# Kernel tuning notes

Hardware: AMD Instinct MI355X
Metric: run time of the kernel (lower is better)

## Reference

```python
import jax, jax.numpy as jnp
import numpy as np

K = 20
EPS = 1e-5

def _lrelu(x):
    return jnp.where(x >= 0, x, 0.2 * x)

def _bn(x, g, b, m, v, axis=1):
    shp = [1] * x.ndim
    shp[axis] = -1
    scale = (g / jnp.sqrt(v + EPS)).reshape(shp)
    return (x - m.reshape(shp)) * scale + b.reshape(shp)

def _graph_feature(x, k):
    # x: [B, C, N] -> [B, 2C, N, k]  (kNN in feature space, concat(x_j - x_i, x_i))
    xx = jnp.sum(x * x, axis=1)                        # [B, N]
    inner = jnp.einsum('bcn,bcm->bnm', x, x)           # [B, N, N]
    neg_dist = 2.0 * inner - xx[:, :, None] - xx[:, None, :]
    _, idx = jax.lax.top_k(neg_dist, k)                # [B, N, k] nearest neighbors
    xt = jnp.transpose(x, (0, 2, 1))                   # [B, N, C]
    nb = jax.vmap(lambda f, i: f[i])(xt, idx)          # [B, N, k, C]
    center = jnp.broadcast_to(xt[:, :, None, :], nb.shape)
    feat = jnp.concatenate([nb - center, center], axis=-1)  # [B, N, k, 2C]
    return jnp.transpose(feat, (0, 3, 1, 2))

def _edge_block(x, w, g, b, m, v):
    # EdgeConv: graph feature -> 1x1 conv -> BN -> LeakyReLU -> max over k
    f = _graph_feature(x, K)                           # [B, 2C, N, k]
    y = jnp.einsum('oc,bcnk->bonk', w, f)
    y = _lrelu(_bn(y, g, b, m, v, 1))
    return jnp.max(y, axis=-1)                         # [B, O, N]


def setup_inputs() -> dict:
    key = jax.random.key(0)
    ks = iter(jax.random.split(key, 64))
    def randn(*s, scale=1.0):
        return jax.random.normal(next(ks), s, dtype=jnp.float32) * scale
    def unif(*s):
        return jax.random.uniform(next(ks), s, dtype=jnp.float32, minval=0.5, maxval=1.5)
    d = {}
    d['x'] = randn(16, 3, 1024)
    # conv / linear weights (fan-in scaled)
    for name, o, c in [('w1', 64, 6), ('w2', 64, 128), ('w3', 128, 128),
                       ('w4', 256, 256), ('w5', 1024, 512),
                       ('wl1', 512, 2048), ('wl2', 256, 512), ('wl3', 101, 256)]:
        d[name] = randn(o, c, scale=1.0 / np.sqrt(c))
    d['bl2'] = randn(256, scale=0.02)
    d['bl3'] = randn(101, scale=0.02)
    # BN params (eval-mode running stats)
    for i, c in [('1', 64), ('2', 64), ('3', 128), ('4', 256), ('5', 1024), ('6', 512), ('7', 256)]:
        d['g' + i] = 1.0 + randn(c, scale=0.1)
        d['b' + i] = randn(c, scale=0.1)
        d['m' + i] = randn(c, scale=0.1)
        d['v' + i] = unif(c)
    return d


def reference(x, w1, g1, b1, m1, v1, w2, g2, b2, m2, v2, w3, g3, b3, m3, v3,
              w4, g4, b4, m4, v4, w5, g5, b5, m5, v5,
              wl1, g6, b6, m6, v6, wl2, bl2, g7, b7, m7, v7, wl3, bl3):
    x1 = _edge_block(x,  w1, g1, b1, m1, v1)   # [B, 64, N]
    x2 = _edge_block(x1, w2, g2, b2, m2, v2)   # [B, 64, N]
    x3 = _edge_block(x2, w3, g3, b3, m3, v3)   # [B, 128, N]
    x4 = _edge_block(x3, w4, g4, b4, m4, v4)   # [B, 256, N]
    xc = jnp.concatenate([x1, x2, x3, x4], axis=1)           # [B, 512, N]
    y = _lrelu(_bn(jnp.einsum('oc,bcn->bon', w5, xc), g5, b5, m5, v5, 1))  # [B, 1024, N]
    p = jnp.concatenate([jnp.max(y, axis=-1), jnp.mean(y, axis=-1)], axis=1)  # [B, 2048]
    h = _lrelu(_bn(p @ wl1.T, g6, b6, m6, v6, 1))            # [B, 512]
    h = _lrelu(_bn(h @ wl2.T + bl2, g7, b7, m7, v7, 1))      # [B, 256]
    return h @ wl3.T + bl3                                   # [B, 101]
```

## Files before the change

kernel.cpp:

```cpp
#include <hip/hip_runtime.h>
#include <cstdint>
#include <cmath>

#define DI __device__ __forceinline__

constexpr int BB = 16;
constexpr int NN = 1024;
constexpr int KK = 20;
constexpr int NPT = BB*NN;
constexpr float EPSF = 1e-5f;
constexpr float NEGINF = -3.0e38f;

DI float lrelu(float x){ return x >= 0.f ? x : 0.2f * x; }
DI float dot4(const float4 a, const float4 b){ return a.x*b.x + a.y*b.y + a.z*b.z + a.w*b.w; }
DI unsigned short f2bf(float x){
    uint32_t u = __float_as_uint(x);
    uint32_t r = (u + 0x7fffu + ((u >> 16) & 1u)) >> 16;
    return (unsigned short)r;
}

DI float wave_max64(float v){
    v = fmaxf(v, __int_as_float(__builtin_amdgcn_mov_dpp(__float_as_int(v), 0x121, 0xF, 0xF, true)));
    v = fmaxf(v, __int_as_float(__builtin_amdgcn_mov_dpp(__float_as_int(v), 0x122, 0xF, 0xF, true)));
    v = fmaxf(v, __int_as_float(__builtin_amdgcn_mov_dpp(__float_as_int(v), 0x124, 0xF, 0xF, true)));
    v = fmaxf(v, __int_as_float(__builtin_amdgcn_mov_dpp(__float_as_int(v), 0x128, 0xF, 0xF, true)));
    v = fmaxf(v, __shfl_xor(v, 16));
    v = fmaxf(v, __shfl_xor(v, 32));
    return v;
}

typedef __attribute__((ext_vector_type(8))) short short8v;
typedef __attribute__((ext_vector_type(4))) float f32x4;

__global__ void k_transpose(const float* __restrict__ x, float* __restrict__ xt)
{
    int i = blockIdx.x * 256 + threadIdx.x;
    if (i >= NPT) return;
    int b = i >> 10, n = i & 1023;
    #pragma unroll
    for (int c = 0; c < 3; ++c) xt[i*3 + c] = x[(b*3 + c)*NN + n];
}

__global__ void k_sqnorm(const float* __restrict__ src, int stride, int C, float* __restrict__ xx)
{
    int i = blockIdx.x * 256 + threadIdx.x;
    if (i >= NPT) return;
    const float* r = src + (size_t)i * stride;
    float s = 0.f;
    for (int c = 0; c < C; ++c){ float v = r[c]; s += v * v; }
    xx[i] = s;
}

template<int C>
__global__ __launch_bounds__(1024, 4) void k_knn(const float* __restrict__ src, int stride,
                                                 const float* __restrict__ xx,
                                                 int* __restrict__ idxo)
{
    constexpr bool SMALL = (C == 3);
    constexpr int CG = SMALL ? 1 : (C / 4);
    constexpr int TS = SMALL ? 5 : C;
    constexpr int NBUF = SMALL ? 1 : 2;
    constexpr int LPT = SMALL ? 1 : (128*CG/1024);
    __shared__ float tile[NBUF][128 * TS];

    const int tid  = threadIdx.x;
    const int lane = tid & 63;
    const int wv   = __builtin_amdgcn_readfirstlane(tid >> 6);
    const int b  = blockIdx.x >> 4;
    const int q0 = (blockIdx.x & 15) << 6;
    const int qbase = b*NN + q0 + (wv << 2);

    const float* qp0 = src + (size_t)(qbase + 0)*stride;
    const float* qp1 = src + (size_t)(qbase + 1)*stride;
    const float* qp2 = src + (size_t)(qbase + 2)*stride;
    const float* qp3 = src + (size_t)(qbase + 3)*stride;

    float xxq[4];
    #pragma unroll
    for (int q = 0; q < 4; ++q) xxq[q] = xx[qbase + q];

    float val[4][16];

    if constexpr (SMALL){
        #pragma unroll
        for (int t = 0; t < 8; ++t){
            __syncthreads();
            for (int i = tid; i < 128*3; i += 1024){
                int row = i / 3, c = i % 3;
                tile[0][row*TS + c] = src[(size_t)(b*NN + t*128 + row)*stride + c];
            }
            __syncthreads();
            float c0a = tile[0][lane*TS+0], c0b = tile[0][lane*TS+1], c0c = tile[0][lane*TS+2];
            float c1a = tile[0][(64+lane)*TS+0], c1b = tile[0][(64+lane)*TS+1], c1c = tile[0][(64+lane)*TS+2];
            float q00 = qp0[0], q01 = qp0[1], q02 = qp0[2];
            float q10 = qp1[0], q11 = qp1[1], q12 = qp1[2];
            float q20 = qp2[0], q21 = qp2[1], q22 = qp2[2];
            float q30 = qp3[0], q31 = qp3[1], q32 = qp3[2];
            float xxm0 = xx[b*NN + t*128 + lane];
            float xxm1 = xx[b*NN + t*128 + 64 + lane];
            val[0][2*t]   = 2.f*(q00*c0a + q01*c0b + q02*c0c) - xxq[0] - xxm0;
            val[0][2*t+1] = 2.f*(q00*c1a + q01*c1b + q02*c1c) - xxq[0] - xxm1;
            val[1][2*t]   = 2.f*(q10*c0a + q11*c0b + q12*c0c) - xxq[1] - xxm0;
            val[1][2*t+1] = 2.f*(q10*c1a + q11*c1b + q12*c1c) - xxq[1] - xxm1;
            val[2][2*t]   = 2.f*(q20*c0a + q21*c0b + q22*c0c) - xxq[2] - xxm0;
            val[2][2*t+1] = 2.f*(q20*c1a + q21*c1b + q22*c1c) - xxq[2] - xxm1;
            val[3][2*t]   = 2.f*(q30*c0a + q31*c0b + q32*c0c) - xxq[3] - xxm0;
            val[3][2*t+1] = 2.f*(q30*c1a + q31*c1b + q32*c1c) - xxq[3] - xxm1;
        }
    } else {
        float4 nx[LPT];
        #pragma unroll
        for (int k = 0; k < LPT; ++k){
            int i = tid + k*1024;
            int row = i / CG, cg = i % CG;
            nx[k] = *(const float4*)(src + (size_t)(b*NN + row)*stride + cg*4);
        }
        #pragma unroll
        for (int k = 0; k < LPT; ++k){
            int i = tid + k*1024;
            int row = i / CG, cg = i % CG;
            int p = cg ^ (row & (CG - 1));
            *(float4*)(&tile[0][row*TS + p*4]) = nx[k];
        }

        for (int t = 0; t < 8; ++t){
            __syncthreads();
            if (t < 7){
                #pragma unroll
                for (int k = 0; k < LPT; ++k){
                    int i = tid + k*1024;
                    int row = i / CG, cg = i % CG;
                    nx[k] = *(const float4*)(src + (size_t)(b*NN + (t+1)*128 + row)*stride + cg*4);
                }
            }
            const float* tb = tile[t & 1];

            float acc[4][2];
            #pragma unroll
            for (int q = 0; q < 4; ++q){ acc[q][0] = 0.f; acc[q][1] = 0.f; }
            const int sw = lane & (CG - 1);
            #pragma unroll 2
            for (int cg0 = 0; cg0 < CG; ++cg0){
                float4 cf0 = *(const float4*)(tb + lane*TS      + ((cg0 ^ sw) << 2));
                float4 cf1 = *(const float4*)(tb + (64+lane)*TS + ((cg0 ^ sw) << 2));
                float4 qf0 = *(const float4*)(qp0 + (cg0 << 2));
                float4 qf1 = *(const float4*)(qp1 + (cg0 << 2));
                float4 qf2 = *(const float4*)(qp2 + (cg0 << 2));
                float4 qf3 = *(const float4*)(qp3 + (cg0 << 2));
                acc[0][0] += dot4(qf0, cf0); acc[0][1] += dot4(qf0, cf1);
                acc[1][0] += dot4(qf1, cf0); acc[1][1] += dot4(qf1, cf1);
                acc[2][0] += dot4(qf2, cf0); acc[2][1] += dot4(qf2, cf1);
                acc[3][0] += dot4(qf3, cf0); acc[3][1] += dot4(qf3, cf1);
            }
            float xxm0 = xx[b*NN + t*128 + lane];
            float xxm1 = xx[b*NN + t*128 + 64 + lane];
            #pragma unroll
            for (int q = 0; q < 4; ++q){
                val[q][2*t]   = 2.f*acc[q][0] - xxq[q] - xxm0;
                val[q][2*t+1] = 2.f*acc[q][1] - xxq[q] - xxm1;
            }

            if (t < 7){
                float* wb = &tile[(t+1) & 1][0];
                #pragma unroll
                for (int k = 0; k < LPT; ++k){
                    int i = tid + k*1024;
                    int row = i / CG, cg = i % CG;
                    int p = cg ^ (row & (CG - 1));
                    *(float4*)(&wb[row*TS + p*4]) = nx[k];
                }
            }
        }
    }

    #pragma unroll
    for (int q = 0; q < 4; ++q){
        const int orow = (qbase + q) * KK;

        float s[16];
        #pragma unroll
        for (int j = 0; j < 16; ++j) s[j] = val[q][j];
        #pragma unroll
        for (int k = 2; k <= 16; k <<= 1){
            #pragma unroll
            for (int jj = k >> 1; jj > 0; jj >>= 1){
                #pragma unroll
                for (int i = 0; i < 16; ++i){
                    int l = i ^ jj;
                    if (l > i){
                        float a = s[i], c = s[l];
                        float mx = fmaxf(a, c), mn = fminf(a, c);
                        bool up = ((i & k) == 0);
                        s[i] = up ? mx : mn;
                        s[l] = up ? mn : mx;
                    }
                }
            }
        }

        float T = NEGINF;
        for (int it = 0; it < 21; ++it){
            float m = wave_max64(s[0]);
            T = m;
            unsigned long long mk = __ballot(s[0] == m);
            int wl = __ffsll(mk) - 1;
            bool adv = (lane == wl);
            #pragma unroll
            for (int j = 0; j < 15; ++j) s[j] = adv ? s[j+1] : s[j];
            s[15] = adv ? NEGINF : s[15];
        }

        int cnt = 0;
        #pragma unroll
        for (int j = 0; j < 16; ++j) cnt += (val[q][j] > T) ? 1 : 0;
        int off = cnt;
        #pragma unroll
        for (int d = 1; d < 64; d <<= 1){
            int tt = __shfl_up(off, d);
            if (lane >= d) off += tt;
        }
        int total = __shfl(off, 63);
        int pos = orow + off - cnt;
        #pragma unroll
        for (int j = 0; j < 16; ++j){
            if (val[q][j] > T){ idxo[pos] = j*64 + lane; ++pos; }
        }
        if (total < KK){
            int rem = KK - total;
            int prior = 0;
            #pragma unroll
            for (int j = 0; j < 16; ++j){
                unsigned long long mk = __ballot(val[q][j] == T);
                int below = __popcll(mk & ((1ull << lane) - 1ull));
                if ((val[q][j] == T) && (prior + below < rem))
                    idxo[orow + total + prior + below] = j*64 + lane;
                prior += __popcll(mk);
            }
        }
    }
}

__global__ void k_wprep(const float* __restrict__ w, int O, int C, float* __restrict__ wp)
{
    int i = blockIdx.x*256 + threadIdx.x;
    if (i >= O*C) return;
    int o = i / C, c = i % C;
    float a = w[o*2*C + c];
    float bq = w[o*2*C + C + c];
    wp[o*C + c]       = a;
    wp[(O + o)*C + c] = bq - a;
}

template<int K, int M2, int O, bool UB16>
__global__ __launch_bounds__(256) void k_uvgemm(const float* __restrict__ srcp,
    const float* __restrict__ wp,
    const float* __restrict__ g, const float* __restrict__ bp,
    const float* __restrict__ mp, const float* __restrict__ vp,
    float* __restrict__ ub, float* __restrict__ xcv)
{
    constexpr int LD = 136;
    __shared__ float wl[16*LD];
    __shared__ float xl[16*LD];
    const int tid = threadIdx.x;
    const int nt = blockIdx.x & 127;
    const int mt = blockIdx.x >> 7;
    const int to = tid >> 4, tn = tid & 15;

    float acc[8][8];
    #pragma unroll
    for (int i = 0; i < 8; ++i)
        #pragma unroll
        for (int j = 0; j < 8; ++j) acc[i][j] = 0.f;

    for (int c0 = 0; c0 < K; c0 += 16){
        __syncthreads();
        #pragma unroll
        for (int p = 0; p < 2; ++p){
            int fi = tid + (p << 8);
            int row = fi >> 2, cq = (fi & 3) << 2;
            float4 wv = *(const float4*)(wp + (size_t)(mt*128 + row)*K + c0 + cq);
            wl[(cq+0)*LD + row] = wv.x;
            wl[(cq+1)*LD + row] = wv.y;
            wl[(cq+2)*LD + row] = wv.z;
            wl[(cq+3)*LD + row] = wv.w;
            float4 xv = *(const float4*)(srcp + (size_t)(nt*128 + row)*512 + c0 + cq);
            xl[(cq+0)*LD + row] = xv.x;
            xl[(cq+1)*LD + row] = xv.y;
            xl[(cq+2)*LD + row] = xv.z;
            xl[(cq+3)*LD + row] = xv.w;
        }
        __syncthreads();
        #pragma unroll
        for (int cc = 0; cc < 16; ++cc){
            float4 a0 = *(const float4*)(wl + cc*LD + to*8);
            float4 a1 = *(const float4*)(wl + cc*LD + to*8 + 4);
            float4 b0 = *(const float4*)(xl + cc*LD + tn*8);
            float4 b1 = *(const float4*)(xl + cc*LD + tn*8 + 4);
            float av[8] = {a0.x,a0.y,a0.z,a0.w,a1.x,a1.y,a1.z,a1.w};
            float bv[8] = {b0.x,b0.y,b0.z,b0.w,b1.x,b1.y,b1.z,b1.w};
            #pragma unroll
            for (int i = 0; i < 8; ++i)
                #pragma unroll
                for (int j = 0; j < 8; ++j) acc[i][j] += av[i]*bv[j];
        }
    }

    const int mbase = mt*128 + to*8;
    const bool isu = mbase < O;
    float mult[8], add[8];
    #pragma unroll
    for (int i = 0; i < 8; ++i){
        int m = mbase + i;
        if (isu){
            float s = g[m] / sqrtf(vp[m] + EPSF);
            mult[i] = (s >= 0.f) ? 1.f : -1.f;
            add[i]  = 0.f;
        } else {
            int o = m - O;
            float s = g[o] / sqrtf(vp[o] + EPSF);
            mult[i] = s;
            add[i]  = bp[o] - mp[o]*s;
        }
    }
    #pragma unroll
    for (int j = 0; j < 8; ++j){
        int pt = nt*128 + tn*8 + j;
        float4 v0, v1;
        v0.x = fmaf(mult[0], acc[0][j], add[0]);
        v0.y = fmaf(mult[1], acc[1][j], add[1]);
        v0.z = fmaf(mult[2], acc[2][j], add[2]);
        v0.w = fmaf(mult[3], acc[3][j], add[3]);
        v1.x = fmaf(mult[4], acc[4][j], add[4]);
        v1.y = fmaf(mult[5], acc[5][j], add[5]);
        v1.z = fmaf(mult[6], acc[6][j], add[6]);
        v1.w = fmaf(mult[7], acc[7][j], add[7]);
        if (isu){
            if constexpr (UB16){
                union { unsigned short u[8]; uint4 v; } o;
                o.u[0] = f2bf(v0.x); o.u[1] = f2bf(v0.y); o.u[2] = f2bf(v0.z); o.u[3] = f2bf(v0.w);
                o.u[4] = f2bf(v1.x); o.u[5] = f2bf(v1.y); o.u[6] = f2bf(v1.z); o.u[7] = f2bf(v1.w);
                *(uint4*)((unsigned short*)ub + (size_t)pt*O + mbase) = o.v;
            } else {
                float* d = ub + (size_t)pt*O + mbase;
                *(float4*)(d)     = v0;
                *(float4*)(d + 4) = v1;
            }
        } else {
            float* d = xcv + (size_t)pt*512 + (mbase - O);
            *(float4*)(d)     = v0;
            *(float4*)(d + 4) = v1;
        }
    }
}

__global__ __launch_bounds__(256) void k_uv3(const float* __restrict__ xt,
    const float* __restrict__ wp,
    const float* __restrict__ g, const float* __restrict__ bp,
    const float* __restrict__ mp, const float* __restrict__ vp,
    float* __restrict__ ub, float* __restrict__ xcv)
{
    __shared__ float wpl[128*3];
    __shared__ float mult[128], add[128];
    const int tid = threadIdx.x;
    if (tid < 128){
        int m = tid;
        if (m < 64){
            float s = g[m] / sqrtf(vp[m] + EPSF);
            mult[m] = (s >= 0.f) ? 1.f : -1.f;
            add[m]  = 0.f;
        } else {
            int o = m - 64;
            float s = g[o] / sqrtf(vp[o] + EPSF);
            mult[m] = s;
            add[m]  = bp[o] - mp[o]*s;
        }
    }
    for (int i = tid; i < 128*3; i += 256) wpl[i] = wp[i];
    __syncthreads();

    const int ptl = tid >> 5, mg = tid & 31;
    const int m0 = mg * 4;
    const int pt = blockIdx.x*8 + ptl;
    float x0 = xt[pt*3+0], x1 = xt[pt*3+1], x2 = xt[pt*3+2];
    float4 v4;
    float tmp[4];
    #pragma unroll
    for (int r = 0; r < 4; ++r){
        int m = m0 + r;
        float a = wpl[m*3+0]*x0 + wpl[m*3+1]*x1 + wpl[m*3+2]*x2;
        tmp[r] = fmaf(mult[m], a, add[m]);
    }
    v4.x = tmp[0]; v4.y = tmp[1]; v4.z = tmp[2]; v4.w = tmp[3];
    if (m0 < 64) *(float4*)(ub + (size_t)pt*64 + m0) = v4;
    else         *(float4*)(xcv + (size_t)pt*512 + (m0 - 64)) = v4;
}

template<int O, bool UB16>
__global__ __launch_bounds__(256) void k_edgemax(const float* __restrict__ ub,
    const int* __restrict__ idxg,
    const float* __restrict__ g, const float* __restrict__ vp,
    float* __restrict__ xcv)
{
    constexpr int TPP = O / 4;
    constexpr int PPB = 256 / TPP;
    const int tid = threadIdx.x;
    const int pt  = blockIdx.x*PPB + tid / TPP;
    const int oq  = (tid % TPP) * 4;
    const int bb  = pt & ~(NN-1);

    int nb[KK];
    #pragma unroll
    for (int k = 0; k < KK; ++k) nb[k] = idxg[pt*KK + k];

    float4 mx;
    if constexpr (UB16){
        const unsigned short* ubh = (const unsigned short*)ub;
        uint2 r0 = *(const uint2*)(ubh + (size_t)(bb + nb[0])*O + oq);
        mx.x = __uint_as_float(r0.x << 16);
        mx.y = __uint_as_float(r0.x & 0xffff0000u);
        mx.z = __uint_as_float(r0.y << 16);
        mx.w = __uint_as_float(r0.y & 0xffff0000u);
        #pragma unroll
        for (int k = 1; k < KK; ++k){
            uint2 r = *(const uint2*)(ubh + (size_t)(bb + nb[k])*O + oq);
            mx.x = fmaxf(mx.x, __uint_as_float(r.x << 16));
            mx.y = fmaxf(mx.y, __uint_as_float(r.x & 0xffff0000u));
            mx.z = fmaxf(mx.z, __uint_as_float(r.y << 16));
            mx.w = fmaxf(mx.w, __uint_as_float(r.y & 0xffff0000u));
        }
    } else {
        mx = *(const float4*)(ub + (size_t)(bb + nb[0])*O + oq);
        #pragma unroll
        for (int k = 1; k < KK; ++k){
            float4 u = *(const float4*)(ub + (size_t)(bb + nb[k])*O + oq);
            mx.x = fmaxf(mx.x, u.x); mx.y = fmaxf(mx.y, u.y);
            mx.z = fmaxf(mx.z, u.z); mx.w = fmaxf(mx.w, u.w);
        }
    }
    float4 gv = *(const float4*)(g + oq);
    float4 vv = *(const float4*)(vp + oq);
    float4 as;
    as.x = fabsf(gv.x / sqrtf(vv.x + EPSF));
    as.y = fabsf(gv.y / sqrtf(vv.y + EPSF));
    as.z = fabsf(gv.z / sqrtf(vv.z + EPSF));
    as.w = fabsf(gv.w / sqrtf(vv.w + EPSF));
    float* d = xcv + (size_t)pt*512 + oq;
    float4 vr = *(const float4*)(d);
    float4 y;
    y.x = lrelu(fmaf(as.x, mx.x, vr.x));
    y.y = lrelu(fmaf(as.y, mx.y, vr.y));
    y.z = lrelu(fmaf(as.z, mx.z, vr.z));
    y.w = lrelu(fmaf(as.w, mx.w, vr.w));
    *(float4*)(d) = y;
}

__global__ void k_castbf(const float* __restrict__ s, unsigned short* __restrict__ d, int n8)
{
    int i = blockIdx.x*256 + threadIdx.x;
    if (i >= n8) return;
    const float4* sp = (const float4*)s + (size_t)i*2;
    float4 a = sp[0], b = sp[1];
    union { unsigned short u[8]; uint4 v; } o;
    o.u[0] = f2bf(a.x); o.u[1] = f2bf(a.y); o.u[2] = f2bf(a.z); o.u[3] = f2bf(a.w);
    o.u[4] = f2bf(b.x); o.u[5] = f2bf(b.y); o.u[6] = f2bf(b.z); o.u[7] = f2bf(b.w);
    *((uint4*)d + i) = o.v;
}

__global__ __launch_bounds__(256) void k_conv5mfma(const unsigned short* __restrict__ xcb,
    const unsigned short* __restrict__ w5b,
    const float* __restrict__ g, const float* __restrict__ bp,
    const float* __restrict__ mp, const float* __restrict__ vp,
    float* __restrict__ pmax, float* __restrict__ psum)
{
    __shared__ __align__(16) short lA[128*32];
    __shared__ __align__(16) short lB[128*32];
    __shared__ float scl[128], adl[128];
    __shared__ float red[2][128][2];

    const int tid = threadIdx.x;
    const int lane = tid & 63, wave = tid >> 6;
    const int wm = wave >> 1, wn = wave & 1;
    const int b  = blockIdx.x >> 6;
    const int mt = (blockIdx.x >> 3) & 7;
    const int nt = blockIdx.x & 7;

    if (tid < 128){
        int o = mt*128 + tid;
        float s = g[o] / sqrtf(vp[o] + EPSF);
        scl[tid] = s;
        adl[tid] = bp[o] - mp[o]*s;
    }

    f32x4 acc[4][4];
    #pragma unroll
    for (int i = 0; i < 4; ++i)
        #pragma unroll
        for (int j = 0; j < 4; ++j) acc[i][j] = (f32x4){0.f,0.f,0.f,0.f};

    const unsigned short* gA = w5b + (size_t)(mt*128)*512;
    const unsigned short* gB = xcb + (size_t)(b*1024 + nt*128)*512;

    for (int ks = 0; ks < 16; ++ks){
        __syncthreads();
        #pragma unroll
        for (int p = 0; p < 2; ++p){
            int off = p*256 + tid;
            int row = off >> 2;
            int slot = off & 3;
            int ssl = slot ^ (row & 3);
            *(uint4*)(lA + row*32 + ssl*8) = *(const uint4*)(gA + (size_t)row*512 + ks*32 + slot*8);
            *(uint4*)(lB + row*32 + ssl*8) = *(const uint4*)(gB + (size_t)row*512 + ks*32 + slot*8);
        }
        __syncthreads();

        short8v afr[4], bfr[4];
        #pragma unroll
        for (int i = 0; i < 4; ++i){
            int row = wm*64 + i*16 + (lane & 15);
            int sl  = (lane >> 4) ^ (row & 3);
            afr[i] = *(const short8v*)(lA + row*32 + sl*8);
        }
        #pragma unroll
        for (int j = 0; j < 4; ++j){
            int row = wn*64 + j*16 + (lane & 15);
            int sl  = (lane >> 4) ^ (row & 3);
            bfr[j] = *(const short8v*)(lB + row*32 + sl*8);
        }
        #pragma unroll
        for (int i = 0; i < 4; ++i)
            #pragma unroll
            for (int j = 0; j < 4; ++j)
                acc[i][j] = __builtin_amdgcn_mfma_f32_16x16x32_bf16(afr[i], bfr[j], acc[i][j], 0, 0, 0);
    }

    float emx[4][4], esm[4][4];
    #pragma unroll
    for (int i = 0; i < 4; ++i){
        #pragma unroll
        for (int r = 0; r < 4; ++r){
            int m_loc = wm*64 + i*16 + (lane >> 4)*4 + r;
            float s = scl[m_loc], t = adl[m_loc];
            float mx = NEGINF, sm = 0.f;
            #pragma unroll
            for (int j = 0; j < 4; ++j){
                float y = lrelu(fmaf(acc[i][j][r], s, t));
                mx = fmaxf(mx, y); sm += y;
            }
            #pragma unroll
            for (int d = 1; d < 16; d <<= 1){
                mx = fmaxf(mx, __shfl_xor(mx, d));
                sm += __shfl_xor(sm, d);
            }
            emx[i][r] = mx; esm[i][r] = sm;
        }
    }
    if ((lane & 15) == 0){
        #pragma unroll
        for (int i = 0; i < 4; ++i)
            #pragma unroll
            for (int r = 0; r < 4; ++r){
                int m_loc = wm*64 + i*16 + (lane >> 4)*4 + r;
                red[wn][m_loc][0] = emx[i][r];
                red[wn][m_loc][1] = esm[i][r];
            }
    }
    __syncthreads();
    if (tid < 128){
        float mx = fmaxf(red[0][tid][0], red[1][tid][0]);
        float sm = red[0][tid][1] + red[1][tid][1];
        int o = mt*128 + tid;
        pmax[(size_t)(b*NN + o)*8 + nt] = mx;
        psum[(size_t)(b*NN + o)*8 + nt] = sm;
    }
}

__global__ void k_poolfin(const float* __restrict__ pmax, const float* __restrict__ psum,
                          float* __restrict__ p)
{
    int i = blockIdx.x*256 + threadIdx.x;
    if (i >= NPT) return;
    int b = i >> 10, o = i & 1023;
    float mx = NEGINF, sm = 0.f;
    #pragma unroll
    for (int t = 0; t < 8; ++t){ mx = fmaxf(mx, pmax[(size_t)i*8 + t]); sm += psum[(size_t)i*8 + t]; }
    p[b*2048 + o]        = mx;
    p[b*2048 + 1024 + o] = sm * (1.f/1024.f);
}

template<int IN, int O, bool HASBN, bool HASBIAS>
__global__ void k_fc(const float* __restrict__ in, const float* __restrict__ W,
                     const float* __restrict__ bias,
                     const float* __restrict__ g, const float* __restrict__ bp,
                     const float* __restrict__ mp, const float* __restrict__ vp,
                     float* __restrict__ out)
{
    int i = blockIdx.x*256 + threadIdx.x;
    if (i >= BB*O) return;
    int b = i / O, o = i % O;
    const float* wr = W  + (size_t)o*IN;
    const float* ir = in + (size_t)b*IN;
    float s = 0.f;
    #pragma unroll 4
    for (int c = 0; c < IN; c += 4){
        float4 a = *(const float4*)(wr + c);
        float4 x = *(const float4*)(ir + c);
        s += dot4(a, x);
    }
    if (HASBIAS) s += bias[o];
    if (HASBN){
        float sc = g[o] / sqrtf(vp[o] + EPSF);
        s = (s - mp[o])*sc + bp[o];
        s = lrelu(s);
    }
    out[(size_t)b*O + o] = s;
}

extern "C" void kernel_launch(void* const* d_in, const int* in_sizes, int n_in,
                              void* d_out, int out_size, void* d_ws, size_t ws_size,
                              hipStream_t stream)
{
    (void)in_sizes; (void)n_in; (void)out_size; (void)ws_size;
    const float* x   = (const float*)d_in[0];
    const float* w1  = (const float*)d_in[1];
    const float* w2  = (const float*)d_in[2];
    const float* w3  = (const float*)d_in[3];
    const float* w4  = (const float*)d_in[4];
    const float* w5  = (const float*)d_in[5];
    const float* wl1 = (const float*)d_in[6];
    const float* wl2 = (const float*)d_in[7];
    const float* wl3 = (const float*)d_in[8];
    const float* bl2 = (const float*)d_in[9];
    const float* bl3 = (const float*)d_in[10];
    const float* g1 = (const float*)d_in[11]; const float* b1 = (const float*)d_in[12];
    const float* m1 = (const float*)d_in[13]; const float* v1 = (const float*)d_in[14];
    const float* g2 = (const float*)d_in[15]; const float* b2 = (const float*)d_in[16];
    const float* m2 = (const float*)d_in[17]; const float* v2 = (const float*)d_in[18];
    const float* g3 = (const float*)d_in[19]; const float* b3 = (const float*)d_in[20];
    const float* m3 = (const float*)d_in[21]; const float* v3 = (const float*)d_in[22];
    const float* g4 = (const float*)d_in[23]; const float* b4 = (const float*)d_in[24];
    const float* m4 = (const float*)d_in[25]; const float* v4 = (const float*)d_in[26];
    const float* g5 = (const float*)d_in[27]; const float* b5 = (const float*)d_in[28];
    const float* m5 = (const float*)d_in[29]; const float* v5 = (const float*)d_in[30];
    const float* g6 = (const float*)d_in[31]; const float* b6 = (const float*)d_in[32];
    const float* m6 = (const float*)d_in[33]; const float* v6 = (const float*)d_in[34];
    const float* g7 = (const float*)d_in[35]; const float* b7 = (const float*)d_in[36];
    const float* m7 = (const float*)d_in[37]; const float* v7 = (const float*)d_in[38];

    float* wsf  = (float*)d_ws;
    float* xt0  = wsf;
    float* xc   = xt0 + 49152;
    float* xx   = xc + 8388608;
    int*   idx  = (int*)(xx + 16384);
    float* pmax = (float*)(idx + 327680);
    float* psum = pmax + 131072;
    float* p    = psum + 131072;
    float* h1   = p + 32768;
    float* h2   = h1 + 8192;
    float* ub   = h2 + 4096;
    float* wp   = ub + 4194304;
    unsigned short* xcb = (unsigned short*)ub;
    unsigned short* w5b = (unsigned short*)idx;

    k_transpose<<<64, 256, 0, stream>>>(x, xt0);

    k_sqnorm<<<64, 256, 0, stream>>>(xt0, 3, 3, xx);
    k_knn<3><<<256, 1024, 0, stream>>>(xt0, 3, xx, idx);
    k_wprep<<<1, 256, 0, stream>>>(w1, 64, 3, wp);
    k_uv3<<<2048, 256, 0, stream>>>(xt0, wp, g1, b1, m1, v1, ub, xc);
    k_edgemax<64, false><<<1024, 256, 0, stream>>>(ub, idx, g1, v1, xc);

    k_sqnorm<<<64, 256, 0, stream>>>(xc, 512, 64, xx);
    k_knn<64><<<256, 1024, 0, stream>>>(xc, 512, xx, idx);
    k_wprep<<<16, 256, 0, stream>>>(w2, 64, 64, wp);
    k_uvgemm<64, 128, 64, false><<<128, 256, 0, stream>>>(xc, wp, g2, b2, m2, v2, ub, xc + 64);
    k_edgemax<64, false><<<1024, 256, 0, stream>>>(ub, idx, g2, v2, xc + 64);

    k_sqnorm<<<64, 256, 0, stream>>>(xc + 64, 512, 64, xx);
    k_knn<64><<<256, 1024, 0, stream>>>(xc + 64, 512, xx, idx);
    k_wprep<<<32, 256, 0, stream>>>(w3, 128, 64, wp);
    k_uvgemm<64, 256, 128, false><<<256, 256, 0, stream>>>(xc + 64, wp, g3, b3, m3, v3, ub, xc + 128);
    k_edgemax<128, false><<<2048, 256, 0, stream>>>(ub, idx, g3, v3, xc + 128);

    k_sqnorm<<<64, 256, 0, stream>>>(xc + 128, 512, 128, xx);
    k_knn<128><<<256, 1024, 0, stream>>>(xc + 128, 512, xx, idx);
    k_wprep<<<128, 256, 0, stream>>>(w4, 256, 128, wp);
    k_uvgemm<128, 512, 256, true><<<512, 256, 0, stream>>>(xc + 128, wp, g4, b4, m4, v4, ub, xc + 256);
    k_edgemax<256, true><<<4096, 256, 0, stream>>>(ub, idx, g4, v4, xc + 256);

    k_castbf<<<4096, 256, 0, stream>>>(xc, xcb, 1048576);
    k_castbf<<<256, 256, 0, stream>>>(w5, w5b, 65536);
    k_conv5mfma<<<1024, 256, 0, stream>>>(xcb, w5b, g5, b5, m5, v5, pmax, psum);
    k_poolfin<<<64, 256, 0, stream>>>(pmax, psum, p);

    k_fc<2048, 512, true,  false><<<32, 256, 0, stream>>>(p,  wl1, nullptr, g6, b6, m6, v6, h1);
    k_fc<512,  256, true,  true ><<<16, 256, 0, stream>>>(h1, wl2, bl2,     g7, b7, m7, v7, h2);
    k_fc<256,  101, false, true ><<<7,  256, 0, stream>>>(h2, wl3, bl3, nullptr, nullptr, nullptr, nullptr, (float*)d_out);
}
```

Before: 581.7 us.

## Fuse sqnorm, weight prep and bf16 casts into neighbouring kernels; MFMA layer-4 GEMM

```diff
diff --git a/kernel.cpp b/kernel.cpp
--- a/kernel.cpp
+++ b/kernel.cpp
@@ -32,23 +32,16 @@
 typedef __attribute__((ext_vector_type(8))) short short8v;
 typedef __attribute__((ext_vector_type(4))) float f32x4;
 
-__global__ void k_transpose(const float* __restrict__ x, float* __restrict__ xt)
+__global__ void k_transpose(const float* __restrict__ x, float* __restrict__ xt, float* __restrict__ xx)
 {
     int i = blockIdx.x * 256 + threadIdx.x;
     if (i >= NPT) return;
     int b = i >> 10, n = i & 1023;
-    #pragma unroll
-    for (int c = 0; c < 3; ++c) xt[i*3 + c] = x[(b*3 + c)*NN + n];
-}
-
-__global__ void k_sqnorm(const float* __restrict__ src, int stride, int C, float* __restrict__ xx)
-{
-    int i = blockIdx.x * 256 + threadIdx.x;
-    if (i >= NPT) return;
-    const float* r = src + (size_t)i * stride;
-    float s = 0.f;
-    for (int c = 0; c < C; ++c){ float v = r[c]; s += v * v; }
-    xx[i] = s;
+    float a = x[(b*3 + 0)*NN + n];
+    float c = x[(b*3 + 1)*NN + n];
+    float d = x[(b*3 + 2)*NN + n];
+    xt[i*3 + 0] = a; xt[i*3 + 1] = c; xt[i*3 + 2] = d;
+    xx[i] = a*a + c*c + d*d;
 }
 
 template<int C>
@@ -240,20 +233,9 @@
     }
 }
 
-__global__ void k_wprep(const float* __restrict__ w, int O, int C, float* __restrict__ wp)
-{
-    int i = blockIdx.x*256 + threadIdx.x;
-    if (i >= O*C) return;
-    int o = i / C, c = i % C;
-    float a = w[o*2*C + c];
-    float bq = w[o*2*C + C + c];
-    wp[o*C + c]       = a;
-    wp[(O + o)*C + c] = bq - a;
-}
-
 template<int K, int M2, int O, bool UB16>
 __global__ __launch_bounds__(256) void k_uvgemm(const float* __restrict__ srcp,
-    const float* __restrict__ wp,
+    const float* __restrict__ w,
     const float* __restrict__ g, const float* __restrict__ bp,
     const float* __restrict__ mp, const float* __restrict__ vp,
     float* __restrict__ ub, float* __restrict__ xcv)
@@ -278,7 +260,16 @@
         for (int p = 0; p < 2; ++p){
             int fi = tid + (p << 8);
             int row = fi >> 2, cq = (fi & 3) << 2;
-            float4 wv = *(const float4*)(wp + (size_t)(mt*128 + row)*K + c0 + cq);
+            int gr = mt*128 + row;
+            float4 wv;
+            if (gr < O){
+                wv = *(const float4*)(w + (size_t)gr*(2*K) + c0 + cq);
+            } else {
+                int o = gr - O;
+                float4 a  = *(const float4*)(w + (size_t)o*(2*K) + c0 + cq);
+                float4 bq = *(const float4*)(w + (size_t)o*(2*K) + K + c0 + cq);
+                wv = make_float4(bq.x-a.x, bq.y-a.y, bq.z-a.z, bq.w-a.w);
+            }
             wl[(cq+0)*LD + row] = wv.x;
             wl[(cq+1)*LD + row] = wv.y;
             wl[(cq+2)*LD + row] = wv.z;
@@ -354,7 +345,7 @@
 }
 
 __global__ __launch_bounds__(256) void k_uv3(const float* __restrict__ xt,
-    const float* __restrict__ wp,
+    const float* __restrict__ w,
     const float* __restrict__ g, const float* __restrict__ bp,
     const float* __restrict__ mp, const float* __restrict__ vp,
     float* __restrict__ ub, float* __restrict__ xcv)
@@ -375,7 +366,10 @@
             add[m]  = bp[o] - mp[o]*s;
         }
     }
-    for (int i = tid; i < 128*3; i += 256) wpl[i] = wp[i];
+    for (int i = tid; i < 128*3; i += 256){
+        int m = i / 3, c = i % 3;
+        wpl[i] = (m < 64) ? w[m*6 + c] : (w[(m-64)*6 + 3 + c] - w[(m-64)*6 + c]);
+    }
     __syncthreads();
 
     const int ptl = tid >> 5, mg = tid & 31;
@@ -395,11 +389,133 @@
     else         *(float4*)(xcv + (size_t)pt*512 + (m0 - 64)) = v4;
 }
 
-template<int O, bool UB16>
+__global__ __launch_bounds__(256) void k_uvmfma(const float* __restrict__ xc,
+    const float* __restrict__ w,
+    const float* __restrict__ g, const float* __restrict__ bp,
+    const float* __restrict__ mp, const float* __restrict__ vp,
+    unsigned short* __restrict__ ub, float* __restrict__ vout)
+{
+    __shared__ __align__(16) short lA[128*32];
+    __shared__ __align__(16) short lB[128*32];
+    __shared__ float scl[128], adl[128];
+
+    const int tid = threadIdx.x;
+    const int lane = tid & 63, wave = tid >> 6;
+    const int wm = wave >> 1, wn = wave & 1;
+    const int mt = blockIdx.x >> 7;
+    const int nt = blockIdx.x & 127;
+
+    if (tid < 128){
+        int m = mt*128 + tid;
+        if (m < 256){
+            float s = g[m] / sqrtf(vp[m] + EPSF);
+            scl[tid] = (s >= 0.f) ? 1.f : -1.f;
+            adl[tid] = 0.f;
+        } else {
+            int o = m - 256;
+            float s = g[o] / sqrtf(vp[o] + EPSF);
+            scl[tid] = s;
+            adl[tid] = bp[o] - mp[o]*s;
+        }
+    }
+
+    f32x4 acc[4][4];
+    #pragma unroll
+    for (int i = 0; i < 4; ++i)
+        #pragma unroll
+        for (int j = 0; j < 4; ++j) acc[i][j] = (f32x4){0.f,0.f,0.f,0.f};
+
+    const bool isu = (mt < 2);
+
+    for (int ks = 0; ks < 4; ++ks){
+        __syncthreads();
+        #pragma unroll
+        for (int p = 0; p < 2; ++p){
+            int off = p*256 + tid;
+            int row = off >> 2;
+            int slot = off & 3;
+            int ssl = slot ^ (row & 3);
+            float va[8];
+            if (isu){
+                int m = mt*128 + row;
+                const float* sp = w + (size_t)m*256 + ks*32 + slot*8;
+                float4 a0 = *(const float4*)(sp);
+                float4 a1 = *(const float4*)(sp + 4);
+                va[0]=a0.x; va[1]=a0.y; va[2]=a0.z; va[3]=a0.w;
+                va[4]=a1.x; va[5]=a1.y; va[6]=a1.z; va[7]=a1.w;
+            } else {
+                int o = (mt-2)*128 + row;
+                const float* sp = w + (size_t)o*256 + ks*32 + slot*8;
+                float4 a0 = *(const float4*)(sp);
+                float4 a1 = *(const float4*)(sp + 4);
+                float4 b0 = *(const float4*)(sp + 128);
+                float4 b1 = *(const float4*)(sp + 132);
+                va[0]=b0.x-a0.x; va[1]=b0.y-a0.y; va[2]=b0.z-a0.z; va[3]=b0.w-a0.w;
+                va[4]=b1.x-a1.x; va[5]=b1.y-a1.y; va[6]=b1.z-a1.z; va[7]=b1.w-a1.w;
+            }
+            union { unsigned short u[8]; uint4 v; } oa;
+            #pragma unroll
+            for (int e = 0; e < 8; ++e) oa.u[e] = f2bf(va[e]);
+            *(uint4*)(lA + row*32 + ssl*8) = oa.v;
+            const float* spb = xc + (size_t)(nt*128 + row)*512 + 128 + ks*32 + slot*8;
+            float4 x0 = *(const float4*)(spb);
+            float4 x1 = *(const float4*)(spb + 4);
+            union { unsigned short u[8]; uint4 v; } ob;
+            ob.u[0]=f2bf(x0.x); ob.u[1]=f2bf(x0.y); ob.u[2]=f2bf(x0.z); ob.u[3]=f2bf(x0.w);
+            ob.u[4]=f2bf(x1.x); ob.u[5]=f2bf(x1.y); ob.u[6]=f2bf(x1.z); ob.u[7]=f2bf(x1.w);
+            *(uint4*)(lB + row*32 + ssl*8) = ob.v;
+        }
+        __syncthreads();
+
+        short8v afr[4], bfr[4];
+        #pragma unroll
+        for (int i = 0; i < 4; ++i){
+            int row = wm*64 + i*16 + (lane & 15);
+            int sl  = (lane >> 4) ^ (row & 3);
+            afr[i] = *(const short8v*)(lA + row*32 + sl*8);
+        }
+        #pragma unroll
+        for (int j = 0; j < 4; ++j){
+            int row = wn*64 + j*16 + (lane & 15);
+            int sl  = (lane >> 4) ^ (row & 3);
+            bfr[j] = *(const short8v*)(lB + row*32 + sl*8);
+        }
+        #pragma unroll
+        for (int i = 0; i < 4; ++i)
+            #pragma unroll
+            for (int j = 0; j < 4; ++j)
+                acc[i][j] = __builtin_amdgcn_mfma_f32_16x16x32_bf16(afr[i], bfr[j], acc[i][j], 0, 0, 0);
+    }
+
+    #pragma unroll
+    for (int i = 0; i < 4; ++i){
+        #pragma unroll
+        for (int j = 0; j < 4; ++j){
+            int m_loc = wm*64 + i*16 + (lane >> 4)*4;
+            int pt    = nt*128 + wn*64 + j*16 + (lane & 15);
+            if (isu){
+                union { unsigned short u[4]; uint2 v; } o;
+                #pragma unroll
+                for (int r = 0; r < 4; ++r)
+                    o.u[r] = f2bf(scl[m_loc + r] * acc[i][j][r]);
+                *(uint2*)(ub + (size_t)pt*256 + mt*128 + m_loc) = o.v;
+            } else {
+                float4 y;
+                y.x = fmaf(scl[m_loc+0], acc[i][j][0], adl[m_loc+0]);
+                y.y = fmaf(scl[m_loc+1], acc[i][j][1], adl[m_loc+1]);
+                y.z = fmaf(scl[m_loc+2], acc[i][j][2], adl[m_loc+2]);
+                y.w = fmaf(scl[m_loc+3], acc[i][j][3], adl[m_loc+3]);
+                *(float4*)(vout + (size_t)pt*512 + (mt-2)*128 + m_loc) = y;
+            }
+        }
+    }
+}
+
+template<int O, bool UB16, bool NORM>
 __global__ __launch_bounds__(256) void k_edgemax(const float* __restrict__ ub,
     const int* __restrict__ idxg,
     const float* __restrict__ g, const float* __restrict__ vp,
-    float* __restrict__ xcv)
+    float* __restrict__ xcv, float* __restrict__ xxout)
 {
     constexpr int TPP = O / 4;
     constexpr int PPB = 256 / TPP;
@@ -452,22 +568,17 @@
     y.z = lrelu(fmaf(as.z, mx.z, vr.z));
     y.w = lrelu(fmaf(as.w, mx.w, vr.w));
     *(float4*)(d) = y;
-}
-
-__global__ void k_castbf(const float* __restrict__ s, unsigned short* __restrict__ d, int n8)
-{
-    int i = blockIdx.x*256 + threadIdx.x;
-    if (i >= n8) return;
-    const float4* sp = (const float4*)s + (size_t)i*2;
-    float4 a = sp[0], b = sp[1];
-    union { unsigned short u[8]; uint4 v; } o;
-    o.u[0] = f2bf(a.x); o.u[1] = f2bf(a.y); o.u[2] = f2bf(a.z); o.u[3] = f2bf(a.w);
-    o.u[4] = f2bf(b.x); o.u[5] = f2bf(b.y); o.u[6] = f2bf(b.z); o.u[7] = f2bf(b.w);
-    *((uint4*)d + i) = o.v;
-}
-
-__global__ __launch_bounds__(256) void k_conv5mfma(const unsigned short* __restrict__ xcb,
-    const unsigned short* __restrict__ w5b,
+
+    if constexpr (NORM){
+        float part = dot4(y, y);
+        #pragma unroll
+        for (int dd = 1; dd < TPP; dd <<= 1) part += __shfl_xor(part, dd);
+        if ((tid & (TPP - 1)) == 0) xxout[pt] = part;
+    }
+}
+
+__global__ __launch_bounds__(256) void k_conv5mfma(const float* __restrict__ xc,
+    const float* __restrict__ w5,
     const float* __restrict__ g, const float* __restrict__ bp,
     const float* __restrict__ mp, const float* __restrict__ vp,
     float* __restrict__ pmax, float* __restrict__ psum)
@@ -497,8 +608,8 @@
         #pragma unroll
         for (int j = 0; j < 4; ++j) acc[i][j] = (f32x4){0.f,0.f,0.f,0.f};
 
-    const unsigned short* gA = w5b + (size_t)(mt*128)*512;
-    const unsigned short* gB = xcb + (size_t)(b*1024 + nt*128)*512;
+    const float* gA = w5 + (size_t)(mt*128)*512;
+    const float* gB = xc + (size_t)(b*1024 + nt*128)*512;
 
     for (int ks = 0; ks < 16; ++ks){
         __syncthreads();
@@ -508,8 +619,20 @@
             int row = off >> 2;
             int slot = off & 3;
             int ssl = slot ^ (row & 3);
-            *(uint4*)(lA + row*32 + ssl*8) = *(const uint4*)(gA + (size_t)row*512 + ks*32 + slot*8);
-            *(uint4*)(lB + row*32 + ssl*8) = *(const uint4*)(gB + (size_t)row*512 + ks*32 + slot*8);
+            const float* spa = gA + (size_t)row*512 + ks*32 + slot*8;
+            float4 a0 = *(const float4*)(spa);
+            float4 a1 = *(const float4*)(spa + 4);
+            union { unsigned short u[8]; uint4 v; } oa;
+            oa.u[0]=f2bf(a0.x); oa.u[1]=f2bf(a0.y); oa.u[2]=f2bf(a0.z); oa.u[3]=f2bf(a0.w);
+            oa.u[4]=f2bf(a1.x); oa.u[5]=f2bf(a1.y); oa.u[6]=f2bf(a1.z); oa.u[7]=f2bf(a1.w);
+            *(uint4*)(lA + row*32 + ssl*8) = oa.v;
+            const float* spb = gB + (size_t)row*512 + ks*32 + slot*8;
+            float4 x0 = *(const float4*)(spb);
+            float4 x1 = *(const float4*)(spb + 4);
+            union { unsigned short u[8]; uint4 v; } ob;
+            ob.u[0]=f2bf(x0.x); ob.u[1]=f2bf(x0.y); ob.u[2]=f2bf(x0.z); ob.u[3]=f2bf(x0.w);
+            ob.u[4]=f2bf(x1.x); ob.u[5]=f2bf(x1.y); ob.u[6]=f2bf(x1.z); ob.u[7]=f2bf(x1.w);
+            *(uint4*)(lB + row*32 + ssl*8) = ob.v;
         }
         __syncthreads();
 
@@ -657,39 +780,26 @@
     float* h1   = p + 32768;
     float* h2   = h1 + 8192;
     float* ub   = h2 + 4096;
-    float* wp   = ub + 4194304;
-    unsigned short* xcb = (unsigned short*)ub;
-    unsigned short* w5b = (unsigned short*)idx;
-
-    k_transpose<<<64, 256, 0, stream>>>(x, xt0);
-
-    k_sqnorm<<<64, 256, 0, stream>>>(xt0, 3, 3, xx);
+
+    k_transpose<<<64, 256, 0, stream>>>(x, xt0, xx);
+
     k_knn<3><<<256, 1024, 0, stream>>>(xt0, 3, xx, idx);
-    k_wprep<<<1, 256, 0, stream>>>(w1, 64, 3, wp);
-    k_uv3<<<2048, 256, 0, stream>>>(xt0, wp, g1, b1, m1, v1, ub, xc);
-    k_edgemax<64, false><<<1024, 256, 0, stream>>>(ub, idx, g1, v1, xc);
-
-    k_sqnorm<<<64, 256, 0, stream>>>(xc, 512, 64, xx);
+    k_uv3<<<2048, 256, 0, stream>>>(xt0, w1, g1, b1, m1, v1, ub, xc);
+    k_edgemax<64, false, true><<<1024, 256, 0, stream>>>(ub, idx, g1, v1, xc, xx);
+
     k_knn<64><<<256, 1024, 0, stream>>>(xc, 512, xx, idx);
-    k_wprep<<<16, 256, 0, stream>>>(w2, 64, 64, wp);
-    k_uvgemm<64, 128, 64, false><<<128, 256, 0, stream>>>(xc, wp, g2, b2, m2, v2, ub, xc + 64);
-    k_edgemax<64, false><<<1024, 256, 0, stream>>>(ub, idx, g2, v2, xc + 64);
-
-    k_sqnorm<<<64, 256, 0, stream>>>(xc + 64, 512, 64, xx);
+    k_uvgemm<64, 128, 64, false><<<128, 256, 0, stream>>>(xc, w2, g2, b2, m2, v2, ub, xc + 64);
+    k_edgemax<64, false, true><<<1024, 256, 0, stream>>>(ub, idx, g2, v2, xc + 64, xx);
+
     k_knn<64><<<256, 1024, 0, stream>>>(xc + 64, 512, xx, idx);
-    k_wprep<<<32, 256, 0, stream>>>(w3, 128, 64, wp);
-    k_uvgemm<64, 256, 128, false><<<256, 256, 0, stream>>>(xc + 64, wp, g3, b3, m3, v3, ub, xc + 128);
-    k_edgemax<128, false><<<2048, 256, 0, stream>>>(ub, idx, g3, v3, xc + 128);
-
-    k_sqnorm<<<64, 256, 0, stream>>>(xc + 128, 512, 128, xx);
+    k_uvgemm<64, 256, 128, false><<<256, 256, 0, stream>>>(xc + 64, w3, g3, b3, m3, v3, ub, xc + 128);
+    k_edgemax<128, false, true><<<2048, 256, 0, stream>>>(ub, idx, g3, v3, xc + 128, xx);
+
     k_knn<128><<<256, 1024, 0, stream>>>(xc + 128, 512, xx, idx);
-    k_wprep<<<128, 256, 0, stream>>>(w4, 256, 128, wp);
-    k_uvgemm<128, 512, 256, true><<<512, 256, 0, stream>>>(xc + 128, wp, g4, b4, m4, v4, ub, xc + 256);
-    k_edgemax<256, true><<<4096, 256, 0, stream>>>(ub, idx, g4, v4, xc + 256);
-
-    k_castbf<<<4096, 256, 0, stream>>>(xc, xcb, 1048576);
-    k_castbf<<<256, 256, 0, stream>>>(w5, w5b, 65536);
-    k_conv5mfma<<<1024, 256, 0, stream>>>(xcb, w5b, g5, b5, m5, v5, pmax, psum);
+    k_uvmfma<<<512, 256, 0, stream>>>(xc, w4, g4, b4, m4, v4, (unsigned short*)ub, xc + 256);
+    k_edgemax<256, true, false><<<4096, 256, 0, stream>>>(ub, idx, g4, v4, xc + 256, nullptr);
+
+    k_conv5mfma<<<1024, 256, 0, stream>>>(xc, w5, g5, b5, m5, v5, pmax, psum);
     k_poolfin<<<64, 256, 0, stream>>>(pmax, psum, p);
 
     k_fc<2048, 512, true,  false><<<32, 256, 0, stream>>>(p,  wl1, nullptr, g6, b6, m6, v6, h1);
```

New measurement: 522.0 us (median of 2 runs). 10.2% less time.
